# Kernel optimization log

Measured on AMD Instinct MI355X. Metric: run time of the kernel, lower is better.

## Reference

```python
import jax, jax.numpy as jnp
import numpy as np

N, E = 100_000, 1_600_000
C_IN = C_OUT = 2


def _ln(h, g, b, eps=1e-5):
    mu = h.mean(-1, keepdims=True)
    var = ((h - mu) ** 2).mean(-1, keepdims=True)
    return (h - mu) * jax.lax.rsqrt(var + eps) * g + b


def _radial(x, W1, b1, g1, be1, W2, b2, g2, be2, W3, b3):
    h = jax.nn.relu(_ln(x @ W1 + b1, g1, be1))
    h = jax.nn.relu(_ln(h @ W2 + b2, g2, be2))
    return h @ W3 + b3


def setup_inputs() -> dict:
    key = jax.random.key(0)
    ks = jax.random.split(key, 20)
    inp = {
        "f0": jax.random.normal(ks[0], (N, C_IN, 1), jnp.float32),
        "f1": jax.random.normal(ks[1], (N, C_IN, 3), jnp.float32),
        "dist": jax.random.uniform(ks[2], (E,), jnp.float32),
        "u": jax.random.randint(ks[3], (E,), 0, N),
        "v": jax.random.randint(ks[4], (E,), 0, N),
        "wq": 0.5 * jax.random.normal(ks[5], (2, C_OUT, C_IN), jnp.float32),
        "wj00": jax.random.normal(ks[6], (E, 1, 1, 1), jnp.float32),
        "wj01": jax.random.normal(ks[7], (E, 1, 1, 3), jnp.float32),
        "wj10": jax.random.normal(ks[8], (E, 1, 3, 1), jnp.float32),
        "wj11": jax.random.normal(ks[9], (E, 3, 3, 3), jnp.float32),
        # radial MLP params for the 4 WLayers, index i = 2*l + k
        "rW1": 0.5 * jax.random.normal(ks[10], (4, C_IN + 1, 16), jnp.float32),
        "rb1": jnp.zeros((4, 16), jnp.float32),
        "g1": jnp.ones((4, 16), jnp.float32),
        "be1": jnp.zeros((4, 16), jnp.float32),
        "rW2": 0.3 * jax.random.normal(ks[11], (4, 16, 16), jnp.float32),
        "rb2": jnp.zeros((4, 16), jnp.float32),
        "g2": jnp.ones((4, 16), jnp.float32),
        "be2": jnp.zeros((4, 16), jnp.float32),
        "W3_00": 0.3 * jax.random.normal(ks[12], (16, 4), jnp.float32),
        "b3_00": jnp.zeros((4,), jnp.float32),
        "W3_01": 0.3 * jax.random.normal(ks[13], (16, 4), jnp.float32),
        "b3_01": jnp.zeros((4,), jnp.float32),
        "W3_10": 0.3 * jax.random.normal(ks[14], (16, 4), jnp.float32),
        "b3_10": jnp.zeros((4,), jnp.float32),
        "W3_11": 0.3 * jax.random.normal(ks[15], (16, 12), jnp.float32),
        "b3_11": jnp.zeros((12,), jnp.float32),
    }
    return inp


def reference(f0, f1, dist, u, v, wq, wj00, wj01, wj10, wj11,
              rW1, rb1, g1, be1, rW2, rb2, g2, be2,
              W3_00, b3_00, W3_01, b3_01, W3_10, b3_10, W3_11, b3_11):
    n = f0.shape[0]
    e = u.shape[0]
    # calc_q: [N, c_out, sum(2k+1)=4]
    q = jnp.concatenate([jnp.einsum('oi,nik->nok', wq[0], f0),
                         jnp.einsum('oi,nik->nok', wq[1], f1)], axis=2)
    # per-edge radial input: [dot(f0_src, f0_dst) over rep dim, dist] -> [E, c_in+1]
    vec = jnp.concatenate([jnp.sum(f0[u] * f0[v], axis=2), dist[:, None]], axis=1)
    f_dst = (f0[v], f1[v])  # edges.dst[k]
    wjs = {(0, 0): wj00, (0, 1): wj01, (1, 0): wj10, (1, 1): wj11}
    W3s = {(0, 0): (W3_00, b3_00), (0, 1): (W3_01, b3_01),
           (1, 0): (W3_10, b3_10), (1, 1): (W3_11, b3_11)}
    # calc_k: for each output degree l, sum over input degrees k of
    #   einsum('ejoi,ejlk,eik->eol', R, w_j, f_dst[k])  (fused form of the
    #   original 'ejoi,ejlk->eoilk' then 'eoilk,eik->eol')
    kl = []
    for l in range(2):
        acc = jnp.zeros((e, C_OUT, 2 * l + 1), f0.dtype)
        for k in range(2):
            i = 2 * l + k
            W3, b3 = W3s[(l, k)]
            J = 2 * min(k, l) + 1
            R = _radial(vec, rW1[i], rb1[i], g1[i], be1[i],
                        rW2[i], rb2[i], g2[i], be2[i], W3, b3)
            R = R.reshape(e, J, C_OUT, C_IN)
            acc = acc + jnp.einsum('ejoi,ejlk,eik->eol', R, wjs[(l, k)], f_dst[k])
        kl.append(acc)
    k_feat = jnp.concatenate(kl, axis=2)  # [E, c_out, 4]
    dot = jnp.einsum('eol,eol->e', q[v], k_feat)  # [E]
    # scatter logsumexp over destination nodes, then edge softmax weights
    m = jax.lax.stop_gradient(jax.ops.segment_max(dot, v, num_segments=n))
    m = jnp.where(jnp.isfinite(m), m, 0.0)
    ssum = jax.ops.segment_sum(jnp.exp(dot - m[v]), v, num_segments=n)
    lse = m + jnp.log(ssum)
    return jnp.exp(dot - lse[v])
```

## Files before the change

kernel.cpp:

```cpp
#include <hip/hip_runtime.h>
#include <math.h>


#define TPB 256

typedef float f2 __attribute__((ext_vector_type(2)));

static __device__ __forceinline__ f2 fma2(f2 a, f2 b, f2 c) {
    return __builtin_elementwise_fma(a, b, c);
}
static __device__ __forceinline__ f2 splat(float x) {
    f2 r;
    r.x = x;
    r.y = x;
    return r;
}
static __device__ __forceinline__ float get16(const f2* h, int c) {
    return (c & 1) ? h[c >> 1].y : h[c >> 1].x;
}

static __device__ __forceinline__ void ln_relu16(f2* h, const float* __restrict__ g,
                                                 const float* __restrict__ be) {
    const f2* g2 = (const f2*)g;
    const f2* be2 = (const f2*)be;
    f2 s = h[0] + h[1] + h[2] + h[3] + h[4] + h[5] + h[6] + h[7];
    const float mu = (s.x + s.y) * 0.0625f;
    const f2 mu2 = splat(mu);
    f2 vs = splat(0.f);
#pragma unroll
    for (int i = 0; i < 8; ++i) {
        f2 d = h[i] - mu2;
        vs = fma2(d, d, vs);
    }
    const float var = (vs.x + vs.y) * 0.0625f;
    const f2 r2 = splat(rsqrtf(var + 1e-5f));
    const f2 zero = splat(0.f);
#pragma unroll
    for (int i = 0; i < 8; ++i) {
        f2 t = (h[i] - mu2) * r2;
        h[i] = __builtin_elementwise_max(fma2(t, g2[i], be2[i]), zero);
    }
}

static __device__ __forceinline__ void radial_h2(
    float v0, float v1, float v2, const float* __restrict__ W1,
    const float* __restrict__ b1, const float* __restrict__ g1,
    const float* __restrict__ be1, const float* __restrict__ W2,
    const float* __restrict__ b2, const float* __restrict__ g2,
    const float* __restrict__ be2, f2* h2) {
    const f2* W1r0 = (const f2*)W1;
    const f2* W1r1 = (const f2*)(W1 + 16);
    const f2* W1r2 = (const f2*)(W1 + 32);
    const f2* b1v = (const f2*)b1;
    const f2 a = splat(v0), b = splat(v1), c = splat(v2);
    f2 h[8];
#pragma unroll
    for (int j = 0; j < 8; ++j)
        h[j] = fma2(a, W1r0[j], fma2(b, W1r1[j], fma2(c, W1r2[j], b1v[j])));
    ln_relu16(h, g1, be1);

    const f2* b2v = (const f2*)b2;
#pragma unroll
    for (int j = 0; j < 8; ++j) h2[j] = b2v[j];
#pragma unroll
    for (int c16 = 0; c16 < 16; ++c16) {
        const f2 hc = splat(get16(h, c16));
        const f2* row = (const f2*)(W2 + c16 * 16);
#pragma unroll
        for (int j = 0; j < 8; ++j) h2[j] = fma2(hc, row[j], h2[j]);
    }
    ln_relu16(h2, g2, be2);
}

static __device__ __forceinline__ void layer3_4(const f2* h2,
                                                const float* __restrict__ W3,
                                                const float* __restrict__ b3,
                                                f2& p0, f2& p1) {
    p0 = *(const f2*)(b3);
    p1 = *(const f2*)(b3 + 2);
#pragma unroll
    for (int c = 0; c < 16; ++c) {
        const f2 hc = splat(get16(h2, c));
        p0 = fma2(hc, *(const f2*)(W3 + c * 4), p0);
        p1 = fma2(hc, *(const f2*)(W3 + c * 4 + 2), p1);
    }
}

__global__ __launch_bounds__(TPB, 2) void edge_kernel(
    const float* __restrict__ f0, const float* __restrict__ f1,
    const float* __restrict__ dist, const int* __restrict__ u,
    const int* __restrict__ v, const float* __restrict__ wq,
    const float* __restrict__ wj00, const float* __restrict__ wj01,
    const float* __restrict__ wj10, const float* __restrict__ wj11,
    const float* __restrict__ rW1, const float* __restrict__ rb1,
    const float* __restrict__ g1, const float* __restrict__ be1,
    const float* __restrict__ rW2, const float* __restrict__ rb2,
    const float* __restrict__ g2, const float* __restrict__ be2,
    const float* __restrict__ W3_00, const float* __restrict__ b3_00,
    const float* __restrict__ W3_01, const float* __restrict__ b3_01,
    const float* __restrict__ W3_10, const float* __restrict__ b3_10,
    const float* __restrict__ W3_11, const float* __restrict__ b3_11,
    float* __restrict__ out, double* __restrict__ ssum, int E) {
    int e = blockIdx.x * blockDim.x + threadIdx.x;
    if (e >= E) return;

    const int uu = u[e];
    const int vv = v[e];

    const float f0u0 = f0[uu * 2 + 0];
    const float f0u1 = f0[uu * 2 + 1];
    const float f0v0 = f0[vv * 2 + 0];
    const float f0v1 = f0[vv * 2 + 1];
    float f1v[2][3];
#pragma unroll
    for (int i = 0; i < 2; ++i)
#pragma unroll
        for (int m = 0; m < 3; ++m) f1v[i][m] = f1[vv * 6 + i * 3 + m];

    const float vec0 = f0u0 * f0v0;
    const float vec1 = f0u1 * f0v1;
    const float vec2 = dist[e];

    float acc0[2] = {0.f, 0.f};
    float acc1[2][3] = {{0.f, 0.f, 0.f}, {0.f, 0.f, 0.f}};

    {
        f2 h2[8];
        radial_h2(vec0, vec1, vec2, rW1 + 0 * 48, rb1 + 0 * 16, g1 + 0 * 16,
                  be1 + 0 * 16, rW2 + 0 * 256, rb2 + 0 * 16, g2 + 0 * 16,
                  be2 + 0 * 16, h2);
        f2 p0, p1;
        layer3_4(h2, W3_00, b3_00, p0, p1);
        const float w = wj00[e];
        acc0[0] += w * (p0.x * f0v0 + p0.y * f0v1);
        acc0[1] += w * (p1.x * f0v0 + p1.y * f0v1);
    }
    {
        f2 h2[8];
        radial_h2(vec0, vec1, vec2, rW1 + 1 * 48, rb1 + 1 * 16, g1 + 1 * 16,
                  be1 + 1 * 16, rW2 + 1 * 256, rb2 + 1 * 16, g2 + 1 * 16,
                  be2 + 1 * 16, h2);
        f2 p0, p1;
        layer3_4(h2, W3_01, b3_01, p0, p1);
        const float w0 = wj01[e * 3 + 0];
        const float w1 = wj01[e * 3 + 1];
        const float w2 = wj01[e * 3 + 2];
        const float s0 = w0 * f1v[0][0] + w1 * f1v[0][1] + w2 * f1v[0][2];
        const float s1 = w0 * f1v[1][0] + w1 * f1v[1][1] + w2 * f1v[1][2];
        acc0[0] += p0.x * s0 + p0.y * s1;
        acc0[1] += p1.x * s0 + p1.y * s1;
    }
    {
        f2 h2[8];
        radial_h2(vec0, vec1, vec2, rW1 + 2 * 48, rb1 + 2 * 16, g1 + 2 * 16,
                  be1 + 2 * 16, rW2 + 2 * 256, rb2 + 2 * 16, g2 + 2 * 16,
                  be2 + 2 * 16, h2);
        f2 p0, p1;
        layer3_4(h2, W3_10, b3_10, p0, p1);
        const float t0 = p0.x * f0v0 + p0.y * f0v1;
        const float t1 = p1.x * f0v0 + p1.y * f0v1;
#pragma unroll
        for (int m = 0; m < 3; ++m) {
            const float w = wj10[e * 3 + m];
            acc1[0][m] += w * t0;
            acc1[1][m] += w * t1;
        }
    }
    {
        f2 h2[8];
        radial_h2(vec0, vec1, vec2, rW1 + 3 * 48, rb1 + 3 * 16, g1 + 3 * 16,
                  be1 + 3 * 16, rW2 + 3 * 256, rb2 + 3 * 16, g2 + 3 * 16,
                  be2 + 3 * 16, h2);
#pragma unroll
        for (int j = 0; j < 3; ++j) {
            f2 p0 = *(const f2*)(b3_11 + j * 4);
            f2 p1 = *(const f2*)(b3_11 + j * 4 + 2);
#pragma unroll
            for (int c = 0; c < 16; ++c) {
                const f2 hc = splat(get16(h2, c));
                p0 = fma2(hc, *(const f2*)(W3_11 + c * 12 + j * 4), p0);
                p1 = fma2(hc, *(const f2*)(W3_11 + c * 12 + j * 4 + 2), p1);
            }
#pragma unroll
            for (int m = 0; m < 3; ++m) {
                const float w0 = wj11[e * 27 + j * 9 + m * 3 + 0];
                const float w1 = wj11[e * 27 + j * 9 + m * 3 + 1];
                const float w2 = wj11[e * 27 + j * 9 + m * 3 + 2];
                const float B0 =
                    w0 * f1v[0][0] + w1 * f1v[0][1] + w2 * f1v[0][2];
                const float B1 =
                    w0 * f1v[1][0] + w1 * f1v[1][1] + w2 * f1v[1][2];
                acc1[0][m] += p0.x * B0 + p0.y * B1;
                acc1[1][m] += p1.x * B0 + p1.y * B1;
            }
        }
    }

    float dot = 0.f;
    {
        const float q00 = wq[0] * f0v0 + wq[1] * f0v1;
        const float q01 = wq[2] * f0v0 + wq[3] * f0v1;
        dot += q00 * acc0[0] + q01 * acc0[1];
#pragma unroll
        for (int m = 0; m < 3; ++m) {
            const float q1m0 = wq[4] * f1v[0][m] + wq[5] * f1v[1][m];
            const float q1m1 = wq[6] * f1v[0][m] + wq[7] * f1v[1][m];
            dot += q1m0 * acc1[0][m] + q1m1 * acc1[1][m];
        }
    }

    out[e] = dot;
    atomicAdd(&ssum[vv], exp((double)dot));
}

__global__ void norm_kernel(float* __restrict__ out, const int* __restrict__ v,
                            const double* __restrict__ ssum, int E) {
    int e = blockIdx.x * blockDim.x + threadIdx.x;
    if (e >= E) return;
    const double t = exp((double)out[e]);
    out[e] = (float)(t / ssum[v[e]]);
}

extern "C" void kernel_launch(void* const* d_in, const int* in_sizes, int n_in,
                              void* d_out, int out_size, void* d_ws,
                              size_t ws_size, hipStream_t stream) {
    const float* f0 = (const float*)d_in[0];
    const float* f1 = (const float*)d_in[1];
    const float* dist = (const float*)d_in[2];
    const int* u = (const int*)d_in[3];
    const int* v = (const int*)d_in[4];
    const float* wq = (const float*)d_in[5];
    const float* wj00 = (const float*)d_in[6];
    const float* wj01 = (const float*)d_in[7];
    const float* wj10 = (const float*)d_in[8];
    const float* wj11 = (const float*)d_in[9];
    const float* rW1 = (const float*)d_in[10];
    const float* rb1 = (const float*)d_in[11];
    const float* g1 = (const float*)d_in[12];
    const float* be1 = (const float*)d_in[13];
    const float* rW2 = (const float*)d_in[14];
    const float* rb2 = (const float*)d_in[15];
    const float* g2 = (const float*)d_in[16];
    const float* be2 = (const float*)d_in[17];
    const float* W3_00 = (const float*)d_in[18];
    const float* b3_00 = (const float*)d_in[19];
    const float* W3_01 = (const float*)d_in[20];
    const float* b3_01 = (const float*)d_in[21];
    const float* W3_10 = (const float*)d_in[22];
    const float* b3_10 = (const float*)d_in[23];
    const float* W3_11 = (const float*)d_in[24];
    const float* b3_11 = (const float*)d_in[25];

    const int N = in_sizes[0] / 2;
    const int E = in_sizes[2];

    double* ssum = (double*)d_ws;
    float* out = (float*)d_out;

    const int ge = (E + TPB - 1) / TPB;

    hipMemsetAsync(ssum, 0, (size_t)N * sizeof(double), stream);
    edge_kernel<<<ge, TPB, 0, stream>>>(
        f0, f1, dist, u, v, wq, wj00, wj01, wj10, wj11, rW1, rb1, g1, be1, rW2,
        rb2, g2, be2, W3_00, b3_00, W3_01, b3_01, W3_10, b3_10, W3_11, b3_11,
        out, ssum, E);
    norm_kernel<<<ge, TPB, 0, stream>>>(out, v, ssum, E);
}
```

Measured before the change: 429.8 us.

## Process two edges per thread and replace double exp with scaled float exp

Each thread now handles two edges, so every weight load from the radial MLPs feeds two FMA streams, and per-edge inputs are read as vectorised nontemporal pairs. The double-precision exp is replaced with a float exp2 split into two power-of-two double scalings, which keeps the wide dynamic range at lower cost. Launch bounds ask for three blocks per CU, and the norm kernel also works on pairs. In exchange, register pressure per thread roughly doubles and the float exp is slightly less accurate than the double one.

New measurement: 430.3 us. About the same (+0.1%).

```diff
diff --git a/kernel.cpp b/kernel.cpp
--- a/kernel.cpp
+++ b/kernel.cpp
@@ -5,6 +5,7 @@
 #define TPB 256
 
 typedef float f2 __attribute__((ext_vector_type(2)));
+typedef int i2 __attribute__((ext_vector_type(2)));
 
 static __device__ __forceinline__ f2 fma2(f2 a, f2 b, f2 c) {
     return __builtin_elementwise_fma(a, b, c);
@@ -19,74 +20,112 @@
     return (c & 1) ? h[c >> 1].y : h[c >> 1].x;
 }
 
-static __device__ __forceinline__ void ln_relu16(f2* h, const float* __restrict__ g,
-                                                 const float* __restrict__ be) {
+static __device__ __forceinline__ double exp_wide(float d) {
+    d = fminf(fmaxf(d, -1400.f), 1400.f);
+    const float t = d * 1.44269504088896340736f;
+    const float k = rintf(t);
+    const float p = exp2f(t - k);
+    const int ik = (int)k;
+    const int k1 = ik >> 1;
+    const int k2 = ik - k1;
+    const double s1 = __hiloint2double((k1 + 1023) << 20, 0);
+    const double s2 = __hiloint2double((k2 + 1023) << 20, 0);
+    return ((double)p * s1) * s2;
+}
+
+static __device__ __forceinline__ void ln_relu16_2(f2 h[2][8],
+                                                   const float* __restrict__ g,
+                                                   const float* __restrict__ be) {
     const f2* g2 = (const f2*)g;
     const f2* be2 = (const f2*)be;
-    f2 s = h[0] + h[1] + h[2] + h[3] + h[4] + h[5] + h[6] + h[7];
-    const float mu = (s.x + s.y) * 0.0625f;
-    const f2 mu2 = splat(mu);
-    f2 vs = splat(0.f);
-#pragma unroll
-    for (int i = 0; i < 8; ++i) {
-        f2 d = h[i] - mu2;
-        vs = fma2(d, d, vs);
-    }
-    const float var = (vs.x + vs.y) * 0.0625f;
-    const f2 r2 = splat(rsqrtf(var + 1e-5f));
-    const f2 zero = splat(0.f);
-#pragma unroll
-    for (int i = 0; i < 8; ++i) {
-        f2 t = (h[i] - mu2) * r2;
-        h[i] = __builtin_elementwise_max(fma2(t, g2[i], be2[i]), zero);
-    }
-}
-
-static __device__ __forceinline__ void radial_h2(
-    float v0, float v1, float v2, const float* __restrict__ W1,
-    const float* __restrict__ b1, const float* __restrict__ g1,
-    const float* __restrict__ be1, const float* __restrict__ W2,
-    const float* __restrict__ b2, const float* __restrict__ g2,
-    const float* __restrict__ be2, f2* h2) {
+#pragma unroll
+    for (int e = 0; e < 2; ++e) {
+        f2 s = h[e][0] + h[e][1] + h[e][2] + h[e][3] + h[e][4] + h[e][5] +
+               h[e][6] + h[e][7];
+        const float mu = (s.x + s.y) * 0.0625f;
+        const f2 mu2 = splat(mu);
+        f2 vs = splat(0.f);
+#pragma unroll
+        for (int i = 0; i < 8; ++i) {
+            f2 dd = h[e][i] - mu2;
+            vs = fma2(dd, dd, vs);
+        }
+        const float var = (vs.x + vs.y) * 0.0625f;
+        const f2 r2 = splat(rsqrtf(var + 1e-5f));
+        const f2 zero = splat(0.f);
+#pragma unroll
+        for (int i = 0; i < 8; ++i) {
+            f2 tt = (h[e][i] - mu2) * r2;
+            h[e][i] = __builtin_elementwise_max(fma2(tt, g2[i], be2[i]), zero);
+        }
+    }
+}
+
+static __device__ __forceinline__ void radial_h2_2(
+    const float* v0, const float* v1, const float* v2,
+    const float* __restrict__ W1, const float* __restrict__ b1,
+    const float* __restrict__ g1, const float* __restrict__ be1,
+    const float* __restrict__ W2, const float* __restrict__ b2,
+    const float* __restrict__ g2, const float* __restrict__ be2,
+    f2 h2[2][8]) {
     const f2* W1r0 = (const f2*)W1;
     const f2* W1r1 = (const f2*)(W1 + 16);
     const f2* W1r2 = (const f2*)(W1 + 32);
     const f2* b1v = (const f2*)b1;
-    const f2 a = splat(v0), b = splat(v1), c = splat(v2);
-    f2 h[8];
-#pragma unroll
-    for (int j = 0; j < 8; ++j)
-        h[j] = fma2(a, W1r0[j], fma2(b, W1r1[j], fma2(c, W1r2[j], b1v[j])));
-    ln_relu16(h, g1, be1);
+    f2 h[2][8];
+#pragma unroll
+    for (int j = 0; j < 8; ++j) {
+        const f2 w0 = W1r0[j], w1 = W1r1[j], w2 = W1r2[j], bb = b1v[j];
+#pragma unroll
+        for (int e = 0; e < 2; ++e)
+            h[e][j] = fma2(splat(v0[e]), w0,
+                           fma2(splat(v1[e]), w1, fma2(splat(v2[e]), w2, bb)));
+    }
+    ln_relu16_2(h, g1, be1);
 
     const f2* b2v = (const f2*)b2;
 #pragma unroll
-    for (int j = 0; j < 8; ++j) h2[j] = b2v[j];
-#pragma unroll
-    for (int c16 = 0; c16 < 16; ++c16) {
-        const f2 hc = splat(get16(h, c16));
-        const f2* row = (const f2*)(W2 + c16 * 16);
-#pragma unroll
-        for (int j = 0; j < 8; ++j) h2[j] = fma2(hc, row[j], h2[j]);
-    }
-    ln_relu16(h2, g2, be2);
-}
-
-static __device__ __forceinline__ void layer3_4(const f2* h2,
-                                                const float* __restrict__ W3,
-                                                const float* __restrict__ b3,
-                                                f2& p0, f2& p1) {
-    p0 = *(const f2*)(b3);
-    p1 = *(const f2*)(b3 + 2);
+    for (int j = 0; j < 8; ++j) {
+        h2[0][j] = b2v[j];
+        h2[1][j] = b2v[j];
+    }
 #pragma unroll
     for (int c = 0; c < 16; ++c) {
-        const f2 hc = splat(get16(h2, c));
-        p0 = fma2(hc, *(const f2*)(W3 + c * 4), p0);
-        p1 = fma2(hc, *(const f2*)(W3 + c * 4 + 2), p1);
-    }
-}
-
-__global__ __launch_bounds__(TPB, 2) void edge_kernel(
+        const f2 hc0 = splat(get16(h[0], c));
+        const f2 hc1 = splat(get16(h[1], c));
+        const f2* row = (const f2*)(W2 + c * 16);
+#pragma unroll
+        for (int j = 0; j < 8; ++j) {
+            const f2 w = row[j];
+            h2[0][j] = fma2(hc0, w, h2[0][j]);
+            h2[1][j] = fma2(hc1, w, h2[1][j]);
+        }
+    }
+    ln_relu16_2(h2, g2, be2);
+}
+
+static __device__ __forceinline__ void layer3_4_2(const f2 h2[2][8],
+                                                  const float* __restrict__ W3,
+                                                  const float* __restrict__ b3,
+                                                  f2* p0, f2* p1) {
+    p0[0] = *(const f2*)(b3);
+    p1[0] = *(const f2*)(b3 + 2);
+    p0[1] = p0[0];
+    p1[1] = p1[0];
+#pragma unroll
+    for (int c = 0; c < 16; ++c) {
+        const f2 wa = *(const f2*)(W3 + c * 4);
+        const f2 wb = *(const f2*)(W3 + c * 4 + 2);
+#pragma unroll
+        for (int e = 0; e < 2; ++e) {
+            const f2 hc = splat(get16(h2[e], c));
+            p0[e] = fma2(hc, wa, p0[e]);
+            p1[e] = fma2(hc, wb, p1[e]);
+        }
+    }
+}
+
+__global__ __launch_bounds__(TPB, 3) void edge_kernel(
     const float* __restrict__ f0, const float* __restrict__ f1,
     const float* __restrict__ dist, const int* __restrict__ u,
     const int* __restrict__ v, const float* __restrict__ wq,
@@ -101,124 +140,199 @@
     const float* __restrict__ W3_10, const float* __restrict__ b3_10,
     const float* __restrict__ W3_11, const float* __restrict__ b3_11,
     float* __restrict__ out, double* __restrict__ ssum, int E) {
-    int e = blockIdx.x * blockDim.x + threadIdx.x;
-    if (e >= E) return;
-
-    const int uu = u[e];
-    const int vv = v[e];
-
-    const float f0u0 = f0[uu * 2 + 0];
-    const float f0u1 = f0[uu * 2 + 1];
-    const float f0v0 = f0[vv * 2 + 0];
-    const float f0v1 = f0[vv * 2 + 1];
-    float f1v[2][3];
-#pragma unroll
-    for (int i = 0; i < 2; ++i)
-#pragma unroll
-        for (int m = 0; m < 3; ++m) f1v[i][m] = f1[vv * 6 + i * 3 + m];
-
-    const float vec0 = f0u0 * f0v0;
-    const float vec1 = f0u1 * f0v1;
-    const float vec2 = dist[e];
-
-    float acc0[2] = {0.f, 0.f};
-    float acc1[2][3] = {{0.f, 0.f, 0.f}, {0.f, 0.f, 0.f}};
+    const int t = blockIdx.x * blockDim.x + threadIdx.x;
+    const int e0 = t * 2;
+    if (e0 >= E) return;
+    const bool has1 = (e0 + 1) < E;
+
+    int ea[2], va_[2];
+    float dd[2], w00[2];
+    if (has1) {
+        const i2 uu2 = __builtin_nontemporal_load((const i2*)u + t);
+        const i2 vv2 = __builtin_nontemporal_load((const i2*)v + t);
+        const f2 dd2 = __builtin_nontemporal_load((const f2*)dist + t);
+        const f2 w002 = __builtin_nontemporal_load((const f2*)wj00 + t);
+        ea[0] = uu2.x;
+        ea[1] = uu2.y;
+        va_[0] = vv2.x;
+        va_[1] = vv2.y;
+        dd[0] = dd2.x;
+        dd[1] = dd2.y;
+        w00[0] = w002.x;
+        w00[1] = w002.y;
+    } else {
+        ea[0] = ea[1] = u[e0];
+        va_[0] = va_[1] = v[e0];
+        dd[0] = dd[1] = dist[e0];
+        w00[0] = w00[1] = wj00[e0];
+    }
+    const int eidx[2] = {e0, has1 ? e0 + 1 : e0};
+
+    float f0u0[2], f0u1[2], f0v0[2], f0v1[2];
+    float f1v[2][2][3];
+#pragma unroll
+    for (int e = 0; e < 2; ++e) {
+        const int uu = ea[e];
+        const int vv = va_[e];
+        f0u0[e] = f0[uu * 2 + 0];
+        f0u1[e] = f0[uu * 2 + 1];
+        f0v0[e] = f0[vv * 2 + 0];
+        f0v1[e] = f0[vv * 2 + 1];
+#pragma unroll
+        for (int i = 0; i < 2; ++i)
+#pragma unroll
+            for (int m = 0; m < 3; ++m) f1v[e][i][m] = f1[vv * 6 + i * 3 + m];
+    }
+
+    float vec0[2], vec1[2], vec2[2];
+#pragma unroll
+    for (int e = 0; e < 2; ++e) {
+        vec0[e] = f0u0[e] * f0v0[e];
+        vec1[e] = f0u1[e] * f0v1[e];
+        vec2[e] = dd[e];
+    }
+
+    float acc0[2][2] = {{0.f, 0.f}, {0.f, 0.f}};
+    float acc1[2][2][3] = {{{0.f}}, {{0.f}}};
 
     {
-        f2 h2[8];
-        radial_h2(vec0, vec1, vec2, rW1 + 0 * 48, rb1 + 0 * 16, g1 + 0 * 16,
-                  be1 + 0 * 16, rW2 + 0 * 256, rb2 + 0 * 16, g2 + 0 * 16,
-                  be2 + 0 * 16, h2);
-        f2 p0, p1;
-        layer3_4(h2, W3_00, b3_00, p0, p1);
-        const float w = wj00[e];
-        acc0[0] += w * (p0.x * f0v0 + p0.y * f0v1);
-        acc0[1] += w * (p1.x * f0v0 + p1.y * f0v1);
+        f2 h2[2][8];
+        radial_h2_2(vec0, vec1, vec2, rW1 + 0 * 48, rb1 + 0 * 16, g1 + 0 * 16,
+                    be1 + 0 * 16, rW2 + 0 * 256, rb2 + 0 * 16, g2 + 0 * 16,
+                    be2 + 0 * 16, h2);
+        f2 p0[2], p1[2];
+        layer3_4_2(h2, W3_00, b3_00, p0, p1);
+#pragma unroll
+        for (int e = 0; e < 2; ++e) {
+            acc0[e][0] += w00[e] * (p0[e].x * f0v0[e] + p0[e].y * f0v1[e]);
+            acc0[e][1] += w00[e] * (p1[e].x * f0v0[e] + p1[e].y * f0v1[e]);
+        }
     }
     {
-        f2 h2[8];
-        radial_h2(vec0, vec1, vec2, rW1 + 1 * 48, rb1 + 1 * 16, g1 + 1 * 16,
-                  be1 + 1 * 16, rW2 + 1 * 256, rb2 + 1 * 16, g2 + 1 * 16,
-                  be2 + 1 * 16, h2);
-        f2 p0, p1;
-        layer3_4(h2, W3_01, b3_01, p0, p1);
-        const float w0 = wj01[e * 3 + 0];
-        const float w1 = wj01[e * 3 + 1];
-        const float w2 = wj01[e * 3 + 2];
-        const float s0 = w0 * f1v[0][0] + w1 * f1v[0][1] + w2 * f1v[0][2];
-        const float s1 = w0 * f1v[1][0] + w1 * f1v[1][1] + w2 * f1v[1][2];
-        acc0[0] += p0.x * s0 + p0.y * s1;
-        acc0[1] += p1.x * s0 + p1.y * s1;
+        f2 h2[2][8];
+        radial_h2_2(vec0, vec1, vec2, rW1 + 1 * 48, rb1 + 1 * 16, g1 + 1 * 16,
+                    be1 + 1 * 16, rW2 + 1 * 256, rb2 + 1 * 16, g2 + 1 * 16,
+                    be2 + 1 * 16, h2);
+        f2 p0[2], p1[2];
+        layer3_4_2(h2, W3_01, b3_01, p0, p1);
+#pragma unroll
+        for (int e = 0; e < 2; ++e) {
+            const float w0 = wj01[eidx[e] * 3 + 0];
+            const float w1 = wj01[eidx[e] * 3 + 1];
+            const float w2 = wj01[eidx[e] * 3 + 2];
+            const float s0 =
+                w0 * f1v[e][0][0] + w1 * f1v[e][0][1] + w2 * f1v[e][0][2];
+            const float s1 =
+                w0 * f1v[e][1][0] + w1 * f1v[e][1][1] + w2 * f1v[e][1][2];
+            acc0[e][0] += p0[e].x * s0 + p0[e].y * s1;
+            acc0[e][1] += p1[e].x * s0 + p1[e].y * s1;
+        }
     }
     {
-        f2 h2[8];
-        radial_h2(vec0, vec1, vec2, rW1 + 2 * 48, rb1 + 2 * 16, g1 + 2 * 16,
-                  be1 + 2 * 16, rW2 + 2 * 256, rb2 + 2 * 16, g2 + 2 * 16,
-                  be2 + 2 * 16, h2);
-        f2 p0, p1;
-        layer3_4(h2, W3_10, b3_10, p0, p1);
-        const float t0 = p0.x * f0v0 + p0.y * f0v1;
-        const float t1 = p1.x * f0v0 + p1.y * f0v1;
+        f2 h2[2][8];
+        radial_h2_2(vec0, vec1, vec2, rW1 + 2 * 48, rb1 + 2 * 16, g1 + 2 * 16,
+                    be1 + 2 * 16, rW2 + 2 * 256, rb2 + 2 * 16, g2 + 2 * 16,
+                    be2 + 2 * 16, h2);
+        f2 p0[2], p1[2];
+        layer3_4_2(h2, W3_10, b3_10, p0, p1);
+#pragma unroll
+        for (int e = 0; e < 2; ++e) {
+            const float t0 = p0[e].x * f0v0[e] + p0[e].y * f0v1[e];
+            const float t1 = p1[e].x * f0v0[e] + p1[e].y * f0v1[e];
+#pragma unroll
+            for (int m = 0; m < 3; ++m) {
+                const float w = wj10[eidx[e] * 3 + m];
+                acc1[e][0][m] += w * t0;
+                acc1[e][1][m] += w * t1;
+            }
+        }
+    }
+    {
+        f2 h2[2][8];
+        radial_h2_2(vec0, vec1, vec2, rW1 + 3 * 48, rb1 + 3 * 16, g1 + 3 * 16,
+                    be1 + 3 * 16, rW2 + 3 * 256, rb2 + 3 * 16, g2 + 3 * 16,
+                    be2 + 3 * 16, h2);
+#pragma unroll
+        for (int j = 0; j < 3; ++j) {
+            f2 p0[2], p1[2];
+            p0[0] = *(const f2*)(b3_11 + j * 4);
+            p1[0] = *(const f2*)(b3_11 + j * 4 + 2);
+            p0[1] = p0[0];
+            p1[1] = p1[0];
+#pragma unroll
+            for (int c = 0; c < 16; ++c) {
+                const f2 wa = *(const f2*)(W3_11 + c * 12 + j * 4);
+                const f2 wb = *(const f2*)(W3_11 + c * 12 + j * 4 + 2);
+#pragma unroll
+                for (int e = 0; e < 2; ++e) {
+                    const f2 hc = splat(get16(h2[e], c));
+                    p0[e] = fma2(hc, wa, p0[e]);
+                    p1[e] = fma2(hc, wb, p1[e]);
+                }
+            }
+#pragma unroll
+            for (int e = 0; e < 2; ++e) {
+#pragma unroll
+                for (int m = 0; m < 3; ++m) {
+                    const float w0 = wj11[eidx[e] * 27 + j * 9 + m * 3 + 0];
+                    const float w1 = wj11[eidx[e] * 27 + j * 9 + m * 3 + 1];
+                    const float w2 = wj11[eidx[e] * 27 + j * 9 + m * 3 + 2];
+                    const float B0 = w0 * f1v[e][0][0] + w1 * f1v[e][0][1] +
+                                     w2 * f1v[e][0][2];
+                    const float B1 = w0 * f1v[e][1][0] + w1 * f1v[e][1][1] +
+                                     w2 * f1v[e][1][2];
+                    acc1[e][0][m] += p0[e].x * B0 + p0[e].y * B1;
+                    acc1[e][1][m] += p1[e].x * B0 + p1[e].y * B1;
+                }
+            }
+        }
+    }
+
+    float dotv[2];
+#pragma unroll
+    for (int e = 0; e < 2; ++e) {
+        float dot = 0.f;
+        const float q00 = wq[0] * f0v0[e] + wq[1] * f0v1[e];
+        const float q01 = wq[2] * f0v0[e] + wq[3] * f0v1[e];
+        dot += q00 * acc0[e][0] + q01 * acc0[e][1];
 #pragma unroll
         for (int m = 0; m < 3; ++m) {
-            const float w = wj10[e * 3 + m];
-            acc1[0][m] += w * t0;
-            acc1[1][m] += w * t1;
-        }
-    }
-    {
-        f2 h2[8];
-        radial_h2(vec0, vec1, vec2, rW1 + 3 * 48, rb1 + 3 * 16, g1 + 3 * 16,
-                  be1 + 3 * 16, rW2 + 3 * 256, rb2 + 3 * 16, g2 + 3 * 16,
-                  be2 + 3 * 16, h2);
-#pragma unroll
-        for (int j = 0; j < 3; ++j) {
-            f2 p0 = *(const f2*)(b3_11 + j * 4);
-            f2 p1 = *(const f2*)(b3_11 + j * 4 + 2);
-#pragma unroll
-            for (int c = 0; c < 16; ++c) {
-                const f2 hc = splat(get16(h2, c));
-                p0 = fma2(hc, *(const f2*)(W3_11 + c * 12 + j * 4), p0);
-                p1 = fma2(hc, *(const f2*)(W3_11 + c * 12 + j * 4 + 2), p1);
-            }
-#pragma unroll
-            for (int m = 0; m < 3; ++m) {
-                const float w0 = wj11[e * 27 + j * 9 + m * 3 + 0];
-                const float w1 = wj11[e * 27 + j * 9 + m * 3 + 1];
-                const float w2 = wj11[e * 27 + j * 9 + m * 3 + 2];
-                const float B0 =
-                    w0 * f1v[0][0] + w1 * f1v[0][1] + w2 * f1v[0][2];
-                const float B1 =
-                    w0 * f1v[1][0] + w1 * f1v[1][1] + w2 * f1v[1][2];
-                acc1[0][m] += p0.x * B0 + p0.y * B1;
-                acc1[1][m] += p1.x * B0 + p1.y * B1;
-            }
-        }
-    }
-
-    float dot = 0.f;
-    {
-        const float q00 = wq[0] * f0v0 + wq[1] * f0v1;
-        const float q01 = wq[2] * f0v0 + wq[3] * f0v1;
-        dot += q00 * acc0[0] + q01 * acc0[1];
-#pragma unroll
-        for (int m = 0; m < 3; ++m) {
-            const float q1m0 = wq[4] * f1v[0][m] + wq[5] * f1v[1][m];
-            const float q1m1 = wq[6] * f1v[0][m] + wq[7] * f1v[1][m];
-            dot += q1m0 * acc1[0][m] + q1m1 * acc1[1][m];
-        }
-    }
-
-    out[e] = dot;
-    atomicAdd(&ssum[vv], exp((double)dot));
+            const float q1m0 = wq[4] * f1v[e][0][m] + wq[5] * f1v[e][1][m];
+            const float q1m1 = wq[6] * f1v[e][0][m] + wq[7] * f1v[e][1][m];
+            dot += q1m0 * acc1[e][0][m] + q1m1 * acc1[e][1][m];
+        }
+        dotv[e] = dot;
+    }
+
+    if (has1) {
+        f2 st;
+        st.x = dotv[0];
+        st.y = dotv[1];
+        __builtin_nontemporal_store(st, (f2*)out + t);
+    } else {
+        out[e0] = dotv[0];
+    }
+    atomicAdd(&ssum[va_[0]], exp_wide(dotv[0]));
+    if (has1) atomicAdd(&ssum[va_[1]], exp_wide(dotv[1]));
 }
 
 __global__ void norm_kernel(float* __restrict__ out, const int* __restrict__ v,
                             const double* __restrict__ ssum, int E) {
-    int e = blockIdx.x * blockDim.x + threadIdx.x;
-    if (e >= E) return;
-    const double t = exp((double)out[e]);
-    out[e] = (float)(t / ssum[v[e]]);
+    const int t = blockIdx.x * blockDim.x + threadIdx.x;
+    const int e0 = t * 2;
+    if (e0 >= E) return;
+    if (e0 + 1 < E) {
+        const f2 dv = __builtin_nontemporal_load((const f2*)out + t);
+        const i2 vv = __builtin_nontemporal_load((const i2*)v + t);
+        const double s0 = ssum[vv.x];
+        const double s1 = ssum[vv.y];
+        f2 r;
+        r.x = (float)(exp_wide(dv.x) / s0);
+        r.y = (float)(exp_wide(dv.y) / s1);
+        __builtin_nontemporal_store(r, (f2*)out + t);
+    } else {
+        out[e0] = (float)(exp_wide(out[e0]) / ssum[v[e0]]);
+    }
 }
 
 extern "C" void kernel_launch(void* const* d_in, const int* in_sizes, int n_in,
@@ -257,12 +371,13 @@
     double* ssum = (double*)d_ws;
     float* out = (float*)d_out;
 
-    const int ge = (E + TPB - 1) / TPB;
+    const int pairs = (E + 1) / 2;
+    const int gp = (pairs + TPB - 1) / TPB;
 
     hipMemsetAsync(ssum, 0, (size_t)N * sizeof(double), stream);
-    edge_kernel<<<ge, TPB, 0, stream>>>(
+    edge_kernel<<<gp, TPB, 0, stream>>>(
         f0, f1, dist, u, v, wq, wj00, wj01, wj10, wj11, rW1, rb1, g1, be1, rW2,
         rb2, g2, be2, W3_00, b3_00, W3_01, b3_01, W3_10, b3_10, W3_11, b3_11,
         out, ssum, E);
-    norm_kernel<<<ge, TPB, 0, stream>>>(out, v, ssum, E);
-}
+    norm_kernel<<<gp, TPB, 0, stream>>>(out, v, ssum, E);
+}
```
